# Kernel optimization log

Measured on AMD Instinct MI355X. Metric: run time of the kernel, lower is better.

## Reference

```python
import jax, jax.numpy as jnp
import numpy as np

B, T, C, H = 2, 2048, 1024, 16
N = C // H
MISS_ROWS = 128


def _rwkv7_scan(q, w_log, k, v, a, b):
    # all [B,T,H,N] float32 (bf16-rounded). RWKV7 delta-rule recurrence:
    #   S_t = S_{t-1} * diag(exp(w_t)) + (S_{t-1} a_t) b_t^T + v_t k_t^T
    #   o_t = S_t q_t   (state S has shape [B,H,Nv,Nk]; decay along k-dim)
    Bq, Tq, Hq, Nq = q.shape

    def step(S, inp):
        q_t, w_t, k_t, v_t, a_t, b_t = inp
        ew = jnp.exp(w_t)  # decay in (0,1) since w_log = -exp(...) < 0
        sa = jnp.einsum('bhvi,bhi->bhv', S, a_t)
        S = S * ew[:, :, None, :] + sa[..., None] * b_t[:, :, None, :] + v_t[..., None] * k_t[:, :, None, :]
        o = jnp.einsum('bhvj,bhj->bhv', S, q_t)
        return S, o

    xs = tuple(jnp.moveaxis(u, 1, 0) for u in (q, w_log, k, v, a, b))
    S0 = jnp.zeros((Bq, Hq, Nq, Nq), jnp.float32)
    _, o = jax.lax.scan(step, S0, xs)
    return jnp.moveaxis(o, 0, 1)  # [B,T,H,N]


def setup_inputs() -> dict:
    key = jax.random.key(0)
    ks = jax.random.split(key, 16)
    f32 = jnp.float32
    return {
        'residual': jax.random.normal(ks[0], (B, T, C), f32),
        'x': jax.random.normal(ks[1], (B, T, C), f32),
        'x0': jax.random.normal(ks[2], (B, T, C), f32),
        'dx0': jax.random.normal(ks[3], (B, T, C), f32),
        'Wq': jax.random.normal(ks[4], (C, C), f32) * 0.02,
        'Wk': jax.random.normal(ks[5], (C, C), f32) * 0.02,
        'Wv': jax.random.normal(ks[6], (C, C), f32) * 0.02,
        'Wproj': jax.random.normal(ks[7], (C, C), f32) * 0.02,
        'x_q': jax.random.uniform(ks[8], (1, 1, C), f32),
        'x_k': jax.random.uniform(ks[9], (1, 1, C), f32),
        'x_v': jax.random.uniform(ks[10], (1, 1, C), f32),
        'v0': 0.7 + 0.1 * jax.random.normal(ks[11], (1, 1, C), f32),
        'w0': -3.0 + 0.5 * jax.random.normal(ks[12], (1, 1, C), f32),
        'a0': 0.1 * jax.random.normal(ks[13], (1, 1, C), f32),
        'miss': jax.random.normal(ks[14], (MISS_ROWS, 4 * C), f32) * 0.02,
        'r_k': 0.1 * jax.random.normal(ks[15], (H, N), f32),
    }


def reference(residual, x, x0, dx0, Wq, Wk, Wv, Wproj, x_q, x_k, x_v, v0, w0, a0, miss, r_k):
    Bx, Tx, Cx = x.shape
    Hh, Nn = r_k.shape
    # token shift: dx_prev = x_{t-1} - x_t (zero-padded at t=0)
    dx_prev = jnp.concatenate([jnp.zeros_like(x[:, :1]), x[:, :-1]], axis=1) - x
    q = (x + dx_prev * x_q) @ Wq.T
    k = (x + dx_prev * x_k) @ Wk.T
    v = (x + dx_prev * x_v) @ Wv.T
    deltas = x[:, :, :miss.shape[0]] @ miss  # [B,T,4C]
    w_delta, v_delta, a_delta, g = jnp.split(deltas, 4, axis=-1)
    log_neglog_w = -jax.nn.softplus(-(w0 + w_delta)) - 0.5
    log_w = -jnp.exp(log_neglog_w)  # log decay, always < 0
    v_first = (x0 + dx0 * x_v) @ Wv.T
    v = v + (v_first - v) * jax.nn.sigmoid(v0 + v_delta)
    g = 1.0 + g
    a = jax.nn.sigmoid(a0 + a_delta)
    kh = k.reshape(Bx, Tx, Hh, Nn)
    kk = kh / jnp.maximum(jnp.linalg.norm(kh, axis=-1, keepdims=True), 1e-12)
    kk = kk.reshape(Bx, Tx, Cx)
    k = k * a
    z = -kk
    b = kk * a
    bf = lambda u: u.astype(jnp.bfloat16).astype(jnp.float32).reshape(Bx, Tx, Hh, Nn)
    qh, wh, kh2, vh, zh, bh = (bf(u) for u in (q, log_w, k, v, z, b))
    y = _rwkv7_scan(qh, wh, kh2, vh, zh, bh) * (float(Nn) ** -0.5)  # [B,T,H,N]
    xnorm = jnp.linalg.norm(x.reshape(Bx, Tx, Hh, Nn), axis=-1, keepdims=True)
    vnorm = jnp.linalg.norm(vh, axis=-1, keepdims=True)
    u = (1.0 - xnorm / (vnorm + 1e-12)) * jax.nn.sigmoid(r_k)
    y = (y + vh * u).reshape(Bx, Tx, Cx)
    y = y * g
    return residual + y @ Wproj.T
```

## Files before the change

kernel.cpp:

```cpp
#include <hip/hip_runtime.h>
#include <stdint.h>
#include <stddef.h>

#define B_ 2
#define T_ 2048
#define C_ 1024
#define H_ 16
#define N_ 64
#define M_ (B_*T_)
#define L_ 128
#define NC_ (T_/L_)

typedef unsigned short ushort_t;
typedef __attribute__((ext_vector_type(8))) __bf16 bf16x8;
typedef __attribute__((ext_vector_type(4))) float  f32x4;

__device__ __forceinline__ ushort_t f2bf(float x){
  uint32_t u = __float_as_uint(x);
  u += 0x7fffu + ((u >> 16) & 1u);
  return (ushort_t)(u >> 16);
}
__device__ __forceinline__ float bf2f(uint32_t hu){
  return __uint_as_float(hu << 16);
}
__device__ __forceinline__ void ldbf16x16(const ushort_t* p, float* o){
  uint4 u0 = *(const uint4*)p;
  uint4 u1 = *(const uint4*)(p+8);
  o[0]=bf2f(u0.x&0xffffu); o[1]=bf2f(u0.x>>16);
  o[2]=bf2f(u0.y&0xffffu); o[3]=bf2f(u0.y>>16);
  o[4]=bf2f(u0.z&0xffffu); o[5]=bf2f(u0.z>>16);
  o[6]=bf2f(u0.w&0xffffu); o[7]=bf2f(u0.w>>16);
  o[8]=bf2f(u1.x&0xffffu); o[9]=bf2f(u1.x>>16);
  o[10]=bf2f(u1.y&0xffffu); o[11]=bf2f(u1.y>>16);
  o[12]=bf2f(u1.z&0xffffu); o[13]=bf2f(u1.z>>16);
  o[14]=bf2f(u1.w&0xffffu); o[15]=bf2f(u1.w>>16);
}
__device__ __forceinline__ float quad_sum(float v){
  float a = __int_as_float(__builtin_amdgcn_mov_dpp(__float_as_int(v), 0xB1, 0xF, 0xF, true));
  v += a;
  float b = __int_as_float(__builtin_amdgcn_mov_dpp(__float_as_int(v), 0x4E, 0xF, 0xF, true));
  return v + b;
}

__device__ __forceinline__ ushort4 mixq4(float4 a, float4 p, float4 c){
  ushort4 o;
  o.x = f2bf(fmaf(p.x - a.x, c.x, a.x));
  o.y = f2bf(fmaf(p.y - a.y, c.y, a.y));
  o.z = f2bf(fmaf(p.z - a.z, c.z, a.z));
  o.w = f2bf(fmaf(p.w - a.w, c.w, a.w));
  return o;
}
__global__ __launch_bounds__(256) void prep_all(
    const float* __restrict__ x, const float* __restrict__ x0,
    const float* __restrict__ dx0,
    const float* __restrict__ xq, const float* __restrict__ xk,
    const float* __restrict__ xv,
    const float* __restrict__ Wq, const float* __restrict__ Wk,
    const float* __restrict__ Wv, const float* __restrict__ Wp,
    const float* __restrict__ miss,
    ushort_t* __restrict__ Aq, ushort_t* __restrict__ Ak,
    ushort_t* __restrict__ Av, ushort_t* __restrict__ Axf,
    ushort_t* __restrict__ Xb,
    ushort_t* __restrict__ Wb, ushort_t* __restrict__ Wpb,
    ushort_t* __restrict__ missT)
{
  __shared__ ushort_t tile[128][66];
  const int blk = blockIdx.x;
  const int tid = threadIdx.x;
  if (blk < 4096){
    const int idx = blk*256 + tid;
    const int col4 = idx & 255;
    const int i = idx >> 8;
    const int t = i & (T_-1);
    float4 a = ((const float4*)x)[idx];
    float4 p = {0.f,0.f,0.f,0.f};
    if (t > 0) p = ((const float4*)x)[idx - 256];
    float4 cq = ((const float4*)xq)[col4];
    float4 ck = ((const float4*)xk)[col4];
    float4 cv = ((const float4*)xv)[col4];
    ((ushort4*)Aq)[idx] = mixq4(a, p, cq);
    ((ushort4*)Ak)[idx] = mixq4(a, p, ck);
    ((ushort4*)Av)[idx] = mixq4(a, p, cv);
    float4 z = ((const float4*)x0)[idx];
    float4 d = ((const float4*)dx0)[idx];
    ushort4 of;
    of.x = f2bf(fmaf(d.x, cv.x, z.x));
    of.y = f2bf(fmaf(d.y, cv.y, z.y));
    of.z = f2bf(fmaf(d.z, cv.z, z.z));
    of.w = f2bf(fmaf(d.w, cv.w, z.w));
    ((ushort4*)Axf)[idx] = of;
    ushort4 ob = {f2bf(a.x), f2bf(a.y), f2bf(a.z), f2bf(a.w)};
    ((ushort4*)Xb)[idx] = ob;
  } else if (blk < 4096 + 5*1024){
    const int y = (blk - 4096) >> 10;
    const float* src = (y==0)?Wq:(y==1)?Wk:(y<4)?Wv:Wp;
    ushort_t* dst = (y<4) ? Wb + (size_t)y*C_*C_ : Wpb;
    const int idx = ((blk - 4096) & 1023)*256 + tid;
    float4 v = ((const float4*)src)[idx];
    ushort4 o = {f2bf(v.x), f2bf(v.y), f2bf(v.z), f2bf(v.w)};
    ((ushort4*)dst)[idx] = o;
  } else {
    const int j0 = (blk - 4096 - 5*1024)*64;
#pragma unroll
    for (int rep=0; rep<8; rep++){
      int k = rep*16 + (tid>>4);
      int jj = (tid&15)*4;
      float4 v = *(const float4*)&miss[(size_t)k*4096 + j0 + jj];
      tile[k][jj+0]=f2bf(v.x); tile[k][jj+1]=f2bf(v.y);
      tile[k][jj+2]=f2bf(v.z); tile[k][jj+3]=f2bf(v.w);
    }
    __syncthreads();
#pragma unroll
    for (int rep=0; rep<8; rep++){
      int j = tid>>2;
      int kk = (tid&3)*32 + rep*4;
      ushort4 o = {tile[kk+0][j], tile[kk+1][j], tile[kk+2][j], tile[kk+3][j]};
      *(ushort4*)&missT[(size_t)(j0+j)*128 + kk] = o;
    }
  }
}

__global__ __launch_bounds__(256, 2) void mfma_gemm(
    const ushort_t* __restrict__ Ab, int lda, int64_t Asz,
    const ushort_t* __restrict__ Bbp, int ldb, int64_t Bsz,
    void* __restrict__ Cb, int ldc, int64_t Csz, int c_bf16,
    const float* __restrict__ resid, int K)
{
  const ushort_t* A  = Ab  + (size_t)blockIdx.z * Asz;
  const ushort_t* Bm = Bbp + (size_t)blockIdx.z * Bsz;
  const int i0 = blockIdx.y * 128;
  const int j0 = blockIdx.x * 128;
  const int tid = threadIdx.x;
  const int lane = tid & 63;
  const int w = tid >> 6;
  const int wm = w & 1, wn = w >> 1;

  __shared__ ushort_t As[128*32];
  __shared__ ushort_t Bs[128*32];

  f32x4 acc[4][4];
#pragma unroll
  for (int i=0;i<4;i++)
#pragma unroll
    for (int j=0;j<4;j++) acc[i][j] = (f32x4){0.f,0.f,0.f,0.f};

  const int lr = lane >> 2;
  const int ls = lane & 3;
  const ushort_t* ga = A  + (size_t)(i0 + w*32 + lr)*lda + ls*8;
  const ushort_t* gb = Bm + (size_t)(j0 + w*32 + lr)*ldb + ls*8;
  const int lm = lane & 15, lq = lane >> 4;

  for (int k0 = 0; k0 < K; k0 += 32){
    __syncthreads();
#pragma unroll
    for (int p=0;p<2;p++){
      __builtin_amdgcn_global_load_lds(
        (const __attribute__((address_space(1))) void*)(ga + (size_t)p*16*lda + k0),
        (__attribute__((address_space(3))) void*)&As[(w*32 + p*16)*32], 16, 0, 0);
      __builtin_amdgcn_global_load_lds(
        (const __attribute__((address_space(1))) void*)(gb + (size_t)p*16*ldb + k0),
        (__attribute__((address_space(3))) void*)&Bs[(w*32 + p*16)*32], 16, 0, 0);
    }
    __syncthreads();
    bf16x8 af[4], bfr[4];
#pragma unroll
    for (int i=0;i<4;i++)
      af[i] = *(const bf16x8*)&As[(wm*64 + i*16 + lm)*32 + lq*8];
#pragma unroll
    for (int j=0;j<4;j++)
      bfr[j] = *(const bf16x8*)&Bs[(wn*64 + j*16 + lm)*32 + lq*8];
#pragma unroll
    for (int i=0;i<4;i++)
#pragma unroll
      for (int j=0;j<4;j++)
        acc[i][j] = __builtin_amdgcn_mfma_f32_16x16x32_bf16(af[i], bfr[j], acc[i][j], 0, 0, 0);
  }

  if (!c_bf16){
    float* C = (float*)Cb + (size_t)blockIdx.z * Csz;
#pragma unroll
    for (int i=0;i<4;i++)
#pragma unroll
      for (int j=0;j<4;j++)
#pragma unroll
        for (int r=0;r<4;r++){
          const int row = i0 + wm*64 + i*16 + lq*4 + r;
          const int col = j0 + wn*64 + j*16 + lm;
          float v = acc[i][j][r];
          if (resid) v += resid[(size_t)row*ldc + col];
          C[(size_t)row*ldc + col] = v;
        }
  } else {
    ushort_t* C = (ushort_t*)Cb + (size_t)blockIdx.z * Csz;
#pragma unroll
    for (int i=0;i<4;i++)
#pragma unroll
      for (int j=0;j<4;j++)
#pragma unroll
        for (int r=0;r<4;r++){
          const int row = i0 + wm*64 + i*16 + lq*4 + r;
          const int col = j0 + wn*64 + j*16 + lm;
          C[(size_t)row*ldc + col] = f2bf(acc[i][j][r]);
        }
  }
}

__global__ __launch_bounds__(256) void fuse_kernel(
    const float* __restrict__ qm, const float* __restrict__ km,
    const float* __restrict__ vm, const float* __restrict__ vfm,
    const ushort_t* __restrict__ del, const float* __restrict__ x,
    const float* __restrict__ w0, const float* __restrict__ v0,
    const float* __restrict__ a0,
    uint32_t* __restrict__ packed, float* __restrict__ gout,
    float* __restrict__ ratio)
{
  const int lane = threadIdx.x & 63;
  const int ht = blockIdx.x*4 + (threadIdx.x >> 6);
  const int i = ht >> 4;
  const int h = ht & 15;
  const int c = h*64 + lane;
  const size_t ic = (size_t)i*C_ + c;
  float qv = qm[ic], kv = km[ic], vv = vm[ic], vfv = vfm[ic], xv = x[ic];
  const size_t d0 = (size_t)i*4*C_ + c;
  float wd = bf2f(del[d0]), vd = bf2f(del[d0+C_]);
  float ad = bf2f(del[d0+2*C_]), gd = bf2f(del[d0+3*C_]);

  float z1 = -(w0[c]+wd);
  float sp = fmaxf(z1, 0.f) + log1pf(expf(-fabsf(z1)));
  float logw = -expf(-sp - 0.5f);
  float sv = 1.f/(1.f+expf(-(v0[c]+vd)));
  vv = vv + (vfv - vv)*sv;
  float gv = 1.f + gd;
  float av = 1.f/(1.f+expf(-(a0[c]+ad)));

  ushort_t vr_u = f2bf(vv);
  float vrf = bf2f(vr_u);

  float ksq = kv*kv, xsq = xv*xv, vsq = vrf*vrf;
#pragma unroll
  for (int off=32; off>0; off>>=1){
    ksq += __shfl_xor(ksq, off, 64);
    xsq += __shfl_xor(xsq, off, 64);
    vsq += __shfl_xor(vsq, off, 64);
  }
  float kn = sqrtf(ksq);
  float kkn = kv / fmaxf(kn, 1e-12f);
  float k2 = kv*av;
  float zv = -kkn;
  float bv = kkn*av;

  uint32_t p0 = (uint32_t)f2bf(logw) | ((uint32_t)f2bf(zv) << 16);
  uint32_t p1 = (uint32_t)f2bf(bv)   | ((uint32_t)f2bf(k2) << 16);
  uint32_t p2 = (uint32_t)f2bf(qv)   | ((uint32_t)vr_u << 16);
  uint32_t* pb = packed + ((size_t)ht*64 + lane)*3;
  pb[0]=p0; pb[1]=p1; pb[2]=p2;
  gout[ic] = gv;
  if (lane == 0)
    ratio[ht] = 1.f - sqrtf(xsq)/(sqrtf(vsq)+1e-12f);
}


__global__ __launch_bounds__(256, 1) void chunk_mdp_kernel(
    const uint32_t* __restrict__ packed,
    float* __restrict__ phi, float* __restrict__ cc, float* __restrict__ md)
{
  const int tid = threadIdx.x;
  const int ch  = tid >> 7;
  const int t7  = tid & 127;
  const int rr  = t7 >> 2;
  const int qr  = t7 & 3;

  __shared__ float    ewS[2][4][N_], vS[2][4][N_];
  __shared__ ushort_t zS[2][4][N_], bS[2][4][N_], qS[2][4][N_], kS[2][4][N_];

  const int gcb = blockIdx.x*2;

  uint32_t pu[2][3];
#pragma unroll
  for (int it=0; it<2; it++){
    int slot = it*256 + tid;
    int sc = slot >> 8, s = (slot >> 6) & 3, d = slot & 63;
    int g = gcb + sc;
    int cx = g & (NC_-1), bh = g >> 4;
    int b = bh >> 4, h = bh & 15;
    size_t ap = (((size_t)(b*T_ + cx*L_ + s))*H_ + h)*64 + d;
    pu[it][0] = packed[ap*3]; pu[it][1] = packed[ap*3+1]; pu[it][2] = packed[ap*3+2];
  }

  float X0[16], X1[16], Z0[16], Z1[16];
#pragma unroll
  for (int i=0;i<16;i++){
    X0[i] = (qr*16+i == 2*rr)   ? 1.f : 0.f;
    X1[i] = (qr*16+i == 2*rr+1) ? 1.f : 0.f;
    Z0[i] = 0.f; Z1[i] = 0.f;
  }

  for (int tg = 0; tg < L_; tg += 4){
    __syncthreads();
#pragma unroll
    for (int it=0; it<2; it++){
      int slot = it*256 + tid;
      int sc = slot >> 8, s = (slot >> 6) & 3, d = slot & 63;
      ewS[sc][s][d] = __expf(bf2f(pu[it][0] & 0xffffu));
      zS[sc][s][d]  = (ushort_t)(pu[it][0] >> 16);
      bS[sc][s][d]  = (ushort_t)(pu[it][1] & 0xffffu);
      kS[sc][s][d]  = (ushort_t)(pu[it][1] >> 16);
      qS[sc][s][d]  = (ushort_t)(pu[it][2] & 0xffffu);
      vS[sc][s][d]  = bf2f(pu[it][2] >> 16);
    }
    if (tg + 4 < L_){
#pragma unroll
      for (int it=0; it<2; it++){
        int slot = it*256 + tid;
        int sc = slot >> 8, s = (slot >> 6) & 3, d = slot & 63;
        int g = gcb + sc;
        int cx = g & (NC_-1), bh = g >> 4;
        int b = bh >> 4, h = bh & 15;
        size_t ap = (((size_t)(b*T_ + cx*L_ + tg+4+s))*H_ + h)*64 + d;
        pu[it][0] = packed[ap*3]; pu[it][1] = packed[ap*3+1]; pu[it][2] = packed[ap*3+2];
      }
    }
    __syncthreads();
#pragma unroll 1
    for (int ss=0; ss<4; ss++){
      float zf[16];
      ldbf16x16(&zS[ch][ss][qr*16], zf);
      float sx0=0.f, sx1=0.f, sz0=0.f, sz1=0.f;
#pragma unroll
      for (int i=0;i<16;i++){
        sx0 = fmaf(X0[i], zf[i], sx0);
        sx1 = fmaf(X1[i], zf[i], sx1);
        sz0 = fmaf(Z0[i], zf[i], sz0);
        sz1 = fmaf(Z1[i], zf[i], sz1);
      }
      sx0 = quad_sum(sx0); sx1 = quad_sum(sx1);
      sz0 = quad_sum(sz0); sz1 = quad_sum(sz1);

      float ef[16], bf[16], qf[16], kf[16];
#pragma unroll
      for (int i4=0;i4<4;i4++)
        *(float4*)&ef[i4*4] = *(const float4*)&ewS[ch][ss][qr*16+i4*4];
      ldbf16x16(&bS[ch][ss][qr*16], bf);
      ldbf16x16(&qS[ch][ss][qr*16], qf);
      ldbf16x16(&kS[ch][ss][qr*16], kf);
      const float v0r = vS[ch][ss][2*rr];
      const float v1r = vS[ch][ss][2*rr+1];

      float m0=0.f,m1=0.f,d0=0.f,d1=0.f;
#pragma unroll
      for (int i=0;i<16;i++){
        float t;
        t = fmaf(X0[i], ef[i], sx0*bf[i]); X0[i]=t; m0 = fmaf(t, qf[i], m0);
        t = fmaf(X1[i], ef[i], sx1*bf[i]); X1[i]=t; m1 = fmaf(t, qf[i], m1);
        t = fmaf(Z0[i], ef[i], fmaf(sz0, bf[i], v0r*kf[i])); Z0[i]=t; d0 = fmaf(t, qf[i], d0);
        t = fmaf(Z1[i], ef[i], fmaf(sz1, bf[i], v1r*kf[i])); Z1[i]=t; d1 = fmaf(t, qf[i], d1);
      }
      m0 = quad_sum(m0); m1 = quad_sum(m1);
      d0 = quad_sum(d0); d1 = quad_sum(d1);
      const size_t mb = ((size_t)(gcb+ch)*L_ + tg+ss)*128;
      if      (qr == 0) md[mb + 2*rr]      = m0;
      else if (qr == 1) md[mb + 2*rr+1]    = m1;
      else if (qr == 2) md[mb + 64 + 2*rr]   = d0;
      else              md[mb + 64 + 2*rr+1] = d1;
    }
  }
  const size_t base = (size_t)(gcb+ch)*4096 + (size_t)(2*rr)*64 + qr*16;
#pragma unroll
  for (int i4=0;i4<4;i4++){
    *(float4*)&phi[base + i4*4]      = (float4){X0[i4*4+0],X0[i4*4+1],X0[i4*4+2],X0[i4*4+3]};
    *(float4*)&phi[base + 64 + i4*4] = (float4){X1[i4*4+0],X1[i4*4+1],X1[i4*4+2],X1[i4*4+3]};
    *(float4*)&cc [base + i4*4]      = (float4){Z0[i4*4+0],Z0[i4*4+1],Z0[i4*4+2],Z0[i4*4+3]};
    *(float4*)&cc [base + 64 + i4*4] = (float4){Z1[i4*4+0],Z1[i4*4+1],Z1[i4*4+2],Z1[i4*4+3]};
  }
}

__global__ __launch_bounds__(256) void chunk_state_kernel(
    const float* __restrict__ phi, const float* __restrict__ cc,
    float* __restrict__ sstart)
{
  const int bh = blockIdx.x;
  const int tid = threadIdx.x;
  const int rb = tid >> 4;
  const int cq = tid & 15;
  __shared__ float Sld[64][65];
  __shared__ float Fld[64][68];
  float acc[4][4];
#pragma unroll
  for (int m=0;m<4;m++)
#pragma unroll
    for (int i=0;i<4;i++) acc[m][i] = 0.f;
#pragma unroll
  for (int m=0;m<4;m++){
    float4 z4 = {0.f,0.f,0.f,0.f};
    *(float4*)&Sld[rb+16*m][cq*4] = z4;
  }
  const float* pc = phi + (size_t)bh*NC_*4096;
  const float* cb = cc  + (size_t)bh*NC_*4096;
  float4 pf[4], pcc[4];
#pragma unroll
  for (int p=0;p<4;p++) pf[p] = *(const float4*)&pc[(size_t)p*1024 + tid*4];
#pragma unroll
  for (int m=0;m<4;m++) pcc[m] = *(const float4*)&cb[(size_t)(rb+16*m)*64 + cq*4];

  for (int c=0;c<NC_;c++){
    __syncthreads();
#pragma unroll
    for (int p=0;p<4;p++){
      int f = p*1024 + tid*4;
      *(float4*)&Fld[f>>6][f&63] = pf[p];
    }
    float na[4][4];
#pragma unroll
    for (int m=0;m<4;m++){
      na[m][0]=pcc[m].x; na[m][1]=pcc[m].y; na[m][2]=pcc[m].z; na[m][3]=pcc[m].w;
    }
#pragma unroll
    for (int m=0;m<4;m++){
      float4 so = {acc[m][0],acc[m][1],acc[m][2],acc[m][3]};
      *(float4*)&sstart[(size_t)(bh*NC_+c)*4096 + (size_t)(rb+16*m)*64 + cq*4] = so;
    }
    if (c+1 < NC_){
#pragma unroll
      for (int p=0;p<4;p++) pf[p] = *(const float4*)&pc[(size_t)(c+1)*4096 + p*1024 + tid*4];
#pragma unroll
      for (int m=0;m<4;m++) pcc[m] = *(const float4*)&cb[(size_t)(c+1)*4096 + (size_t)(rb+16*m)*64 + cq*4];
    }
    __syncthreads();
#pragma unroll 1
    for (int k0=0;k0<64;k0+=4){
      float4 sr[4];
#pragma unroll
      for (int m=0;m<4;m++) sr[m] = *(const float4*)&Sld[rb+16*m][k0];
      const float4 f0 = *(const float4*)&Fld[k0+0][cq*4];
      const float4 f1 = *(const float4*)&Fld[k0+1][cq*4];
      const float4 f2 = *(const float4*)&Fld[k0+2][cq*4];
      const float4 f3 = *(const float4*)&Fld[k0+3][cq*4];
#pragma unroll
      for (int m=0;m<4;m++){
        na[m][0] = fmaf(sr[m].x, f0.x, na[m][0]); na[m][0] = fmaf(sr[m].y, f1.x, na[m][0]);
        na[m][0] = fmaf(sr[m].z, f2.x, na[m][0]); na[m][0] = fmaf(sr[m].w, f3.x, na[m][0]);
        na[m][1] = fmaf(sr[m].x, f0.y, na[m][1]); na[m][1] = fmaf(sr[m].y, f1.y, na[m][1]);
        na[m][1] = fmaf(sr[m].z, f2.y, na[m][1]); na[m][1] = fmaf(sr[m].w, f3.y, na[m][1]);
        na[m][2] = fmaf(sr[m].x, f0.z, na[m][2]); na[m][2] = fmaf(sr[m].y, f1.z, na[m][2]);
        na[m][2] = fmaf(sr[m].z, f2.z, na[m][2]); na[m][2] = fmaf(sr[m].w, f3.z, na[m][2]);
        na[m][3] = fmaf(sr[m].x, f0.w, na[m][3]); na[m][3] = fmaf(sr[m].y, f1.w, na[m][3]);
        na[m][3] = fmaf(sr[m].z, f2.w, na[m][3]); na[m][3] = fmaf(sr[m].w, f3.w, na[m][3]);
      }
    }
    __syncthreads();
#pragma unroll
    for (int m=0;m<4;m++){
      float4 so = {na[m][0],na[m][1],na[m][2],na[m][3]};
      *(float4*)&Sld[rb+16*m][cq*4] = so;
#pragma unroll
      for (int i=0;i<4;i++) acc[m][i] = na[m][i];
    }
  }
}

__global__ __launch_bounds__(256) void chunk_emit_kernel(
    const uint32_t* __restrict__ packed, const float* __restrict__ ratio,
    const float* __restrict__ g, const float* __restrict__ rk,
    const float* __restrict__ sstart, const float* __restrict__ md,
    ushort_t* __restrict__ y)
{
  const int blk = blockIdx.x;
  const int c  = blk & (NC_-1);
  const int bh = blk >> 4;
  const int b = bh >> 4, h = bh & 15;
  const int tid = threadIdx.x;
  const int v = tid & 63;
  const int tg = tid >> 6;

  float4 sr[16];
  const float4* sp = (const float4*)(sstart + (size_t)blk*4096 + (size_t)v*64);
#pragma unroll
  for (int f=0;f<16;f++) sr[f] = sp[f];
  const float sigrk = 1.f/(1.f+__expf(-rk[h*64+v]));

#pragma unroll 1
  for (int ss=0; ss<32; ss++){
    const int t = tg*32 + ss;
    const int token = b*T_ + c*L_ + t;
    const float* mrow = md + ((size_t)blk*L_ + t)*128;
    float o0=0.f,o1=0.f,o2=0.f,o3=0.f;
#pragma unroll
    for (int f=0;f<16;f+=4){
      float4 m0 = ((const float4*)mrow)[f+0];
      float4 m1 = ((const float4*)mrow)[f+1];
      float4 m2 = ((const float4*)mrow)[f+2];
      float4 m3 = ((const float4*)mrow)[f+3];
      o0 = fmaf(sr[f+0].x,m0.x, fmaf(sr[f+0].y,m0.y, fmaf(sr[f+0].z,m0.z, fmaf(sr[f+0].w,m0.w, o0))));
      o1 = fmaf(sr[f+1].x,m1.x, fmaf(sr[f+1].y,m1.y, fmaf(sr[f+1].z,m1.z, fmaf(sr[f+1].w,m1.w, o1))));
      o2 = fmaf(sr[f+2].x,m2.x, fmaf(sr[f+2].y,m2.y, fmaf(sr[f+2].z,m2.z, fmaf(sr[f+2].w,m2.w, o2))));
      o3 = fmaf(sr[f+3].x,m3.x, fmaf(sr[f+3].y,m3.y, fmaf(sr[f+3].z,m3.z, fmaf(sr[f+3].w,m3.w, o3))));
    }
    float o = ((o0+o1)+(o2+o3)) + mrow[64 + v];
    const float vt = bf2f(packed[(((size_t)token*H_ + h)*64 + v)*3 + 2] >> 16);
    const float uv = ratio[(size_t)token*H_ + h];
    const float gv = g[(size_t)token*C_ + h*64 + v];
    y[(size_t)token*C_ + h*64 + v] = f2bf((o*0.125f + vt*uv*sigrk)*gv);
  }
}

extern "C" void kernel_launch(void* const* d_in, const int* in_sizes, int n_in,
                              void* d_out, int out_size, void* d_ws, size_t ws_size,
                              hipStream_t stream)
{
  const float* residual = (const float*)d_in[0];
  const float* x    = (const float*)d_in[1];
  const float* x0   = (const float*)d_in[2];
  const float* dx0  = (const float*)d_in[3];
  const float* Wq   = (const float*)d_in[4];
  const float* Wk   = (const float*)d_in[5];
  const float* Wv   = (const float*)d_in[6];
  const float* Wpr  = (const float*)d_in[7];
  const float* x_q  = (const float*)d_in[8];
  const float* x_k  = (const float*)d_in[9];
  const float* x_v  = (const float*)d_in[10];
  const float* v0   = (const float*)d_in[11];
  const float* w0   = (const float*)d_in[12];
  const float* a0   = (const float*)d_in[13];
  const float* miss = (const float*)d_in[14];
  const float* rk   = (const float*)d_in[15];
  float* out = (float*)d_out;

  char* ws = (char*)d_ws;
  const size_t MB = (size_t)1 << 20;
  float*    q_m    = (float*)(ws + 0*MB);
  float*    k_m    = (float*)(ws + 16*MB);
  float*    v_m    = (float*)(ws + 32*MB);
  float*    vf_m   = (float*)(ws + 48*MB);
  ushort_t* delb   = (ushort_t*)(ws + 64*MB);
  ushort_t* Ab     = (ushort_t*)(ws + 96*MB);
  ushort_t* Xb     = (ushort_t*)(ws + 128*MB);
  ushort_t* Wb     = (ushort_t*)(ws + 136*MB);
  uint32_t* packed = (uint32_t*)(ws + 96*MB);
  float*    g_m    = (float*)(ws + 144*MB);
  ushort_t* Wpb    = (ushort_t*)(ws + 160*MB);
  ushort_t* missT  = (ushort_t*)(ws + 162*MB);
  float*    ratio  = (float*)(ws + 163*MB);
  float*    phi    = (float*)(ws + 0*MB);
  float*    cc     = (float*)(ws + 16*MB);
  float*    sstart = (float*)(ws + 32*MB);
  ushort_t* yb     = (ushort_t*)(ws + 48*MB);
  float*    mdbuf  = (float*)(ws + 64*MB);

  ushort_t* Aq  = Ab + 0*(size_t)M_*C_;
  ushort_t* Ak  = Ab + 1*(size_t)M_*C_;
  ushort_t* Av  = Ab + 2*(size_t)M_*C_;
  ushort_t* Axf = Ab + 3*(size_t)M_*C_;

  dim3 blk(256);
  prep_all<<<4096 + 5*1024 + 64, blk, 0, stream>>>(
      x, x0, dx0, x_q, x_k, x_v, Wq, Wk, Wv, Wpr, miss,
      Aq, Ak, Av, Axf, Xb, Wb, Wpb, missT);
  mfma_gemm<<<dim3(C_/128, M_/128, 4), blk, 0, stream>>>(
      Ab, C_, (int64_t)M_*C_, Wb, C_, (int64_t)C_*C_,
      q_m, C_, (int64_t)M_*C_, 0, nullptr, C_);
  mfma_gemm<<<dim3(4*C_/128, M_/128, 1), blk, 0, stream>>>(
      Xb, C_, 0, missT, 128, 0, delb, 4*C_, 0, 1, nullptr, 128);
  fuse_kernel<<<M_*H_/4, blk, 0, stream>>>(q_m, k_m, v_m, vf_m, delb, x, w0, v0, a0, packed, g_m, ratio);
  chunk_mdp_kernel<<<B_*H_*NC_/2, blk, 0, stream>>>(packed, phi, cc, mdbuf);
  chunk_state_kernel<<<B_*H_, blk, 0, stream>>>(phi, cc, sstart);
  chunk_emit_kernel<<<B_*H_*NC_, blk, 0, stream>>>(packed, ratio, g_m, rk, sstart, mdbuf, yb);
  mfma_gemm<<<dim3(C_/128, M_/128, 1), blk, 0, stream>>>(
      yb, C_, 0, Wpb, C_, 0, out, C_, 0, 0, residual, C_);
}
```

Measured before the change: 531.8 us.

## Split chunk_mdp work across 512 threads with one row per thread

Restructures the chunk transition kernel so each block handles a single chunk with 512 threads. The first half of the block tracks the transition (phi) rows and the second half tracks the inhomogeneous (cc) rows, with one state row per thread instead of two. Staged inputs are now stored as float in shared memory and eight timesteps are loaded per sync instead of four. This halves per-thread serial work and register state and doubles the grid, aiming to raise occupancy and shorten the serial critical path, at the cost of more blocks and a larger shared-memory footprint.

```diff
diff --git a/kernel.cpp b/kernel.cpp
--- a/kernel.cpp
+++ b/kernel.cpp
@@ -260,118 +260,108 @@
 }
 
 
-__global__ __launch_bounds__(256, 1) void chunk_mdp_kernel(
+__global__ __launch_bounds__(512, 4) void chunk_mdp_kernel(
     const uint32_t* __restrict__ packed,
     float* __restrict__ phi, float* __restrict__ cc, float* __restrict__ md)
 {
-  const int tid = threadIdx.x;
-  const int ch  = tid >> 7;
-  const int t7  = tid & 127;
-  const int rr  = t7 >> 2;
-  const int qr  = t7 & 3;
-
-  __shared__ float    ewS[2][4][N_], vS[2][4][N_];
-  __shared__ ushort_t zS[2][4][N_], bS[2][4][N_], qS[2][4][N_], kS[2][4][N_];
-
-  const int gcb = blockIdx.x*2;
-
-  uint32_t pu[2][3];
-#pragma unroll
-  for (int it=0; it<2; it++){
-    int slot = it*256 + tid;
-    int sc = slot >> 8, s = (slot >> 6) & 3, d = slot & 63;
-    int g = gcb + sc;
-    int cx = g & (NC_-1), bh = g >> 4;
-    int b = bh >> 4, h = bh & 15;
-    size_t ap = (((size_t)(b*T_ + cx*L_ + s))*H_ + h)*64 + d;
-    pu[it][0] = packed[ap*3]; pu[it][1] = packed[ap*3+1]; pu[it][2] = packed[ap*3+2];
-  }
-
-  float X0[16], X1[16], Z0[16], Z1[16];
-#pragma unroll
-  for (int i=0;i<16;i++){
-    X0[i] = (qr*16+i == 2*rr)   ? 1.f : 0.f;
-    X1[i] = (qr*16+i == 2*rr+1) ? 1.f : 0.f;
-    Z0[i] = 0.f; Z1[i] = 0.f;
-  }
-
-  for (int tg = 0; tg < L_; tg += 4){
-    __syncthreads();
-#pragma unroll
-    for (int it=0; it<2; it++){
-      int slot = it*256 + tid;
-      int sc = slot >> 8, s = (slot >> 6) & 3, d = slot & 63;
-      ewS[sc][s][d] = __expf(bf2f(pu[it][0] & 0xffffu));
-      zS[sc][s][d]  = (ushort_t)(pu[it][0] >> 16);
-      bS[sc][s][d]  = (ushort_t)(pu[it][1] & 0xffffu);
-      kS[sc][s][d]  = (ushort_t)(pu[it][1] >> 16);
-      qS[sc][s][d]  = (ushort_t)(pu[it][2] & 0xffffu);
-      vS[sc][s][d]  = bf2f(pu[it][2] >> 16);
-    }
-    if (tg + 4 < L_){
-#pragma unroll
-      for (int it=0; it<2; it++){
-        int slot = it*256 + tid;
-        int sc = slot >> 8, s = (slot >> 6) & 3, d = slot & 63;
-        int g = gcb + sc;
-        int cx = g & (NC_-1), bh = g >> 4;
-        int b = bh >> 4, h = bh & 15;
-        size_t ap = (((size_t)(b*T_ + cx*L_ + tg+4+s))*H_ + h)*64 + d;
-        pu[it][0] = packed[ap*3]; pu[it][1] = packed[ap*3+1]; pu[it][2] = packed[ap*3+2];
+  const int tid  = threadIdx.x;
+  const int role = tid >> 8;
+  const int row  = (tid >> 2) & 63;
+  const int qr   = tid & 3;
+
+  __shared__ float ewS[8][N_], zS[8][N_], bS[8][N_], kS[8][N_], qS[8][N_], vS[8][N_];
+
+  const int g  = blockIdx.x;
+  const int cx = g & (NC_-1), bh = g >> 4;
+  const int b = bh >> 4, h = bh & 15;
+  const size_t pbase = ((size_t)(b*T_ + cx*L_)*H_ + h)*64;
+
+  const int ls = tid >> 6;
+  const int ld = tid & 63;
+
+  uint32_t pu0, pu1, pu2;
+  {
+    size_t ap = (pbase + (size_t)ls*(H_*64) + ld)*3;
+    pu0 = packed[ap]; pu1 = packed[ap+1]; pu2 = packed[ap+2];
+  }
+
+  float R[16];
+  if (role == 0){
+#pragma unroll
+    for (int i=0;i<16;i++) R[i] = (qr*16+i == row) ? 1.f : 0.f;
+  } else {
+#pragma unroll
+    for (int i=0;i<16;i++) R[i] = 0.f;
+  }
+
+  for (int tg = 0; tg < L_; tg += 8){
+    __syncthreads();
+    ewS[ls][ld] = __expf(bf2f(pu0 & 0xffffu));
+    zS[ls][ld]  = bf2f(pu0 >> 16);
+    bS[ls][ld]  = bf2f(pu1 & 0xffffu);
+    kS[ls][ld]  = bf2f(pu1 >> 16);
+    qS[ls][ld]  = bf2f(pu2 & 0xffffu);
+    vS[ls][ld]  = bf2f(pu2 >> 16);
+    if (tg + 8 < L_){
+      size_t ap = (pbase + (size_t)(tg+8+ls)*(H_*64) + ld)*3;
+      pu0 = packed[ap]; pu1 = packed[ap+1]; pu2 = packed[ap+2];
+    }
+    __syncthreads();
+#pragma unroll 1
+    for (int ss=0; ss<8; ss++){
+      const float* zr = &zS[ss][qr*16];
+      float s_ = 0.f;
+#pragma unroll
+      for (int i4=0;i4<4;i4++){
+        float4 z4 = *(const float4*)&zr[i4*4];
+        s_ = fmaf(R[i4*4+0], z4.x, s_);
+        s_ = fmaf(R[i4*4+1], z4.y, s_);
+        s_ = fmaf(R[i4*4+2], z4.z, s_);
+        s_ = fmaf(R[i4*4+3], z4.w, s_);
       }
-    }
-    __syncthreads();
-#pragma unroll 1
-    for (int ss=0; ss<4; ss++){
-      float zf[16];
-      ldbf16x16(&zS[ch][ss][qr*16], zf);
-      float sx0=0.f, sx1=0.f, sz0=0.f, sz1=0.f;
-#pragma unroll
-      for (int i=0;i<16;i++){
-        sx0 = fmaf(X0[i], zf[i], sx0);
-        sx1 = fmaf(X1[i], zf[i], sx1);
-        sz0 = fmaf(Z0[i], zf[i], sz0);
-        sz1 = fmaf(Z1[i], zf[i], sz1);
+      s_ = quad_sum(s_);
+      const float* er = &ewS[ss][qr*16];
+      const float* br = &bS[ss][qr*16];
+      const float* qrp = &qS[ss][qr*16];
+      float o = 0.f;
+      if (role == 0){
+#pragma unroll
+        for (int i4=0;i4<4;i4++){
+          float4 e4 = *(const float4*)&er[i4*4];
+          float4 b4 = *(const float4*)&br[i4*4];
+          float4 q4 = *(const float4*)&qrp[i4*4];
+          float t;
+          t = fmaf(R[i4*4+0], e4.x, s_*b4.x); R[i4*4+0]=t; o = fmaf(t, q4.x, o);
+          t = fmaf(R[i4*4+1], e4.y, s_*b4.y); R[i4*4+1]=t; o = fmaf(t, q4.y, o);
+          t = fmaf(R[i4*4+2], e4.z, s_*b4.z); R[i4*4+2]=t; o = fmaf(t, q4.z, o);
+          t = fmaf(R[i4*4+3], e4.w, s_*b4.w); R[i4*4+3]=t; o = fmaf(t, q4.w, o);
+        }
+      } else {
+        const float* kr = &kS[ss][qr*16];
+        const float vr = vS[ss][row];
+#pragma unroll
+        for (int i4=0;i4<4;i4++){
+          float4 e4 = *(const float4*)&er[i4*4];
+          float4 b4 = *(const float4*)&br[i4*4];
+          float4 q4 = *(const float4*)&qrp[i4*4];
+          float4 k4 = *(const float4*)&kr[i4*4];
+          float t;
+          t = fmaf(R[i4*4+0], e4.x, fmaf(s_, b4.x, vr*k4.x)); R[i4*4+0]=t; o = fmaf(t, q4.x, o);
+          t = fmaf(R[i4*4+1], e4.y, fmaf(s_, b4.y, vr*k4.y)); R[i4*4+1]=t; o = fmaf(t, q4.y, o);
+          t = fmaf(R[i4*4+2], e4.z, fmaf(s_, b4.z, vr*k4.z)); R[i4*4+2]=t; o = fmaf(t, q4.z, o);
+          t = fmaf(R[i4*4+3], e4.w, fmaf(s_, b4.w, vr*k4.w)); R[i4*4+3]=t; o = fmaf(t, q4.w, o);
+        }
       }
-      sx0 = quad_sum(sx0); sx1 = quad_sum(sx1);
-      sz0 = quad_sum(sz0); sz1 = quad_sum(sz1);
-
-      float ef[16], bf[16], qf[16], kf[16];
-#pragma unroll
-      for (int i4=0;i4<4;i4++)
-        *(float4*)&ef[i4*4] = *(const float4*)&ewS[ch][ss][qr*16+i4*4];
-      ldbf16x16(&bS[ch][ss][qr*16], bf);
-      ldbf16x16(&qS[ch][ss][qr*16], qf);
-      ldbf16x16(&kS[ch][ss][qr*16], kf);
-      const float v0r = vS[ch][ss][2*rr];
-      const float v1r = vS[ch][ss][2*rr+1];
-
-      float m0=0.f,m1=0.f,d0=0.f,d1=0.f;
-#pragma unroll
-      for (int i=0;i<16;i++){
-        float t;
-        t = fmaf(X0[i], ef[i], sx0*bf[i]); X0[i]=t; m0 = fmaf(t, qf[i], m0);
-        t = fmaf(X1[i], ef[i], sx1*bf[i]); X1[i]=t; m1 = fmaf(t, qf[i], m1);
-        t = fmaf(Z0[i], ef[i], fmaf(sz0, bf[i], v0r*kf[i])); Z0[i]=t; d0 = fmaf(t, qf[i], d0);
-        t = fmaf(Z1[i], ef[i], fmaf(sz1, bf[i], v1r*kf[i])); Z1[i]=t; d1 = fmaf(t, qf[i], d1);
-      }
-      m0 = quad_sum(m0); m1 = quad_sum(m1);
-      d0 = quad_sum(d0); d1 = quad_sum(d1);
-      const size_t mb = ((size_t)(gcb+ch)*L_ + tg+ss)*128;
-      if      (qr == 0) md[mb + 2*rr]      = m0;
-      else if (qr == 1) md[mb + 2*rr+1]    = m1;
-      else if (qr == 2) md[mb + 64 + 2*rr]   = d0;
-      else              md[mb + 64 + 2*rr+1] = d1;
-    }
-  }
-  const size_t base = (size_t)(gcb+ch)*4096 + (size_t)(2*rr)*64 + qr*16;
-#pragma unroll
-  for (int i4=0;i4<4;i4++){
-    *(float4*)&phi[base + i4*4]      = (float4){X0[i4*4+0],X0[i4*4+1],X0[i4*4+2],X0[i4*4+3]};
-    *(float4*)&phi[base + 64 + i4*4] = (float4){X1[i4*4+0],X1[i4*4+1],X1[i4*4+2],X1[i4*4+3]};
-    *(float4*)&cc [base + i4*4]      = (float4){Z0[i4*4+0],Z0[i4*4+1],Z0[i4*4+2],Z0[i4*4+3]};
-    *(float4*)&cc [base + 64 + i4*4] = (float4){Z1[i4*4+0],Z1[i4*4+1],Z1[i4*4+2],Z1[i4*4+3]};
-  }
+      o = quad_sum(o);
+      if (qr == 0)
+        md[((size_t)g*L_ + tg+ss)*128 + role*64 + row] = o;
+    }
+  }
+  float* dst = (role == 0) ? phi : cc;
+  const size_t base = (size_t)g*4096 + (size_t)row*64 + qr*16;
+#pragma unroll
+  for (int i4=0;i4<4;i4++)
+    *(float4*)&dst[base + i4*4] = (float4){R[i4*4+0],R[i4*4+1],R[i4*4+2],R[i4*4+3]};
 }
 
 __global__ __launch_bounds__(256) void chunk_state_kernel(
@@ -561,7 +551,7 @@
   mfma_gemm<<<dim3(4*C_/128, M_/128, 1), blk, 0, stream>>>(
       Xb, C_, 0, missT, 128, 0, delb, 4*C_, 0, 1, nullptr, 128);
   fuse_kernel<<<M_*H_/4, blk, 0, stream>>>(q_m, k_m, v_m, vf_m, delb, x, w0, v0, a0, packed, g_m, ratio);
-  chunk_mdp_kernel<<<B_*H_*NC_/2, blk, 0, stream>>>(packed, phi, cc, mdbuf);
+  chunk_mdp_kernel<<<B_*H_*NC_, dim3(512), 0, stream>>>(packed, phi, cc, mdbuf);
   chunk_state_kernel<<<B_*H_, blk, 0, stream>>>(phi, cc, sstart);
   chunk_emit_kernel<<<B_*H_*NC_, blk, 0, stream>>>(packed, ratio, g_m, rk, sstart, mdbuf, yb);
   mfma_gemm<<<dim3(C_/128, M_/128, 1), blk, 0, stream>>>(
```

Measured after the change: 507.6 us. 1.05x faster.
